# Optimization experiments

Hardware: AMD Instinct MI355X
Metric: run time of the kernel (lower is better)

Reference implementation:

```python
import jax, jax.numpy as jnp
import numpy as np

IN_SHAPE = 4096
H_S = 250        # sender_hidden
H_R = 100        # receiver_hidden
MAX_LEN = 30     # message_shape[0]
VOCAB = 40       # message_shape[1]; EOS = VOCAB-1
OUT_CLS = 512 ** 2  # out_shape[1] ** out_shape[0]


def lstm_cell(x, h, c, W_ih, W_hh, b_ih, b_hh):
    # PyTorch LSTM cell: gate order i, f, g, o
    gates = W_ih @ x + b_ih + W_hh @ h + b_hh
    i, f, g, o = jnp.split(gates, 4)
    c_new = jax.nn.sigmoid(f) * c + jax.nn.sigmoid(i) * jnp.tanh(g)
    h_new = jax.nn.sigmoid(o) * jnp.tanh(c_new)
    return h_new, c_new


def setup_inputs() -> dict:
    key = jax.random.key(0)
    ks = jax.random.split(key, 16)
    s = 0.05
    return {
        "x": jax.random.normal(ks[0], (IN_SHAPE,), dtype=jnp.float32),
        "gumbel_noise": jax.random.gumbel(ks[1], (MAX_LEN, VOCAB), dtype=jnp.float32),
        "W_s1": jax.random.normal(ks[2], (H_S, IN_SHAPE)) * s,
        "b_s1": jnp.zeros((H_S,), jnp.float32),
        "W_ih1": jax.random.normal(ks[3], (4 * H_S, VOCAB)) * s,
        "W_hh1": jax.random.normal(ks[4], (4 * H_S, H_S)) * s,
        "b_ih1": jnp.zeros((4 * H_S,), jnp.float32),
        "b_hh1": jnp.zeros((4 * H_S,), jnp.float32),
        "W_p": jax.random.normal(ks[5], (VOCAB, H_S)) * s,
        "b_p": jnp.zeros((VOCAB,), jnp.float32),
        "W_ih2": jax.random.normal(ks[6], (4 * H_R, VOCAB)) * s,
        "W_hh2": jax.random.normal(ks[7], (4 * H_R, H_R)) * s,
        "b_ih2": jnp.zeros((4 * H_R,), jnp.float32),
        "b_hh2": jnp.zeros((4 * H_R,), jnp.float32),
        "W_r": jax.random.normal(ks[8], (OUT_CLS, H_R)) * s,
        "b_r": jnp.zeros((OUT_CLS,), jnp.float32),
    }


def reference(x, gumbel_noise, W_s1, b_s1, W_ih1, W_hh1, b_ih1, b_hh1,
              W_p, b_p, W_ih2, W_hh2, b_ih2, b_hh2, W_r, b_r):
    dt = x.dtype
    eos = jax.nn.one_hot(VOCAB - 1, VOCAB, dtype=dt)
    # sender: h0 = relu(sender1(x)), c0 = 0, first input = sos = zeros
    h0 = jax.nn.relu(W_s1 @ x + b_s1)
    c0 = jnp.zeros((H_S,), dt)
    sos = jnp.zeros((VOCAB,), dt)
    is_last = jnp.arange(MAX_LEN) == MAX_LEN - 1

    def sender_step(carry, inp):
        h, c, sym, done = carry
        g, last = inp
        nh, nc = lstm_cell(sym, h, c, W_ih1, W_hh1, b_ih1, b_hh1)
        logits = W_p @ nh + b_p
        soft = jax.nn.softmax(logits + g)  # gumbel_softmax, tau=1
        idx = jnp.argmax(soft)
        hard = jax.nn.one_hot(idx, VOCAB, dtype=dt)
        st = hard + soft - jax.lax.stop_gradient(soft)  # straight-through
        # at max length the original appends the plain EOS constant
        emit = jnp.where(last & ~done, eos, st)
        emit = jnp.where(done, eos, emit)
        valid = ~done  # this symbol is part of the message
        new_done = done | (idx == VOCAB - 1) | last
        h = jnp.where(done, h, nh)
        c = jnp.where(done, c, nc)
        sym = jnp.where(done, sym, emit)
        return (h, c, sym, new_done), (emit, valid)

    _, (msg, valid) = jax.lax.scan(
        sender_step, (h0, c0, sos, jnp.array(False)), (gumbel_noise, is_last))

    # receiver LSTM: consume message up to and including first EOS (freeze after)
    def recv_step(carry, inp):
        h, c = carry
        sym, v = inp
        nh, nc = lstm_cell(sym, h, c, W_ih2, W_hh2, b_ih2, b_hh2)
        return (jnp.where(v, nh, h), jnp.where(v, nc, c)), None

    (hR, _), _ = jax.lax.scan(
        recv_step, (jnp.zeros((H_R,), dt), jnp.zeros((H_R,), dt)), (msg, valid))
    return jax.nn.softmax(W_r @ hR + b_r)  # [OUT_CLS]
```

## Files before the change

kernel.cpp:

```cpp
#include <hip/hip_runtime.h>
#include <math.h>

#define HS    250
#define HRr   100
#define VOC   40
#define TMAX  30
#define NCLS  262144
#define KS    10
#define RPB   25

typedef unsigned long long ull;

#define PKNH(wsp, par) ((ull*)(wsp) + (size_t)(par) * 256)
#define PKLP(wsp, par) ((ull*)(wsp) + 512 + (size_t)(par) * 400)
#define PKMSG(wsp)     ((ull*)(wsp) + 1312)
#define WS_SUMS 5024
#define WS_HR   5088
#define WS_ZERO_BYTES 20352

#define AST(p, v) __hip_atomic_store((p), (v), __ATOMIC_RELAXED, __HIP_MEMORY_SCOPE_AGENT)
#define ALD(p)    __hip_atomic_load((p), __ATOMIC_RELAXED, __HIP_MEMORY_SCOPE_AGENT)

__device__ __forceinline__ float sigf(float x) { return 1.f / (1.f + expf(-x)); }
__device__ __forceinline__ float lanebc(float v, int l) {
  return __int_as_float(__builtin_amdgcn_readlane(__float_as_int(v), l));
}
__device__ __forceinline__ ull packtv(unsigned tag, float v) {
  return ((ull)tag << 32) | (ull)__float_as_uint(v);
}
__device__ __forceinline__ float lowf(ull w) { return __uint_as_float((unsigned)w); }

#define SENDER_GATES(P, HV)                                   \
  {                                                           \
    _Pragma("unroll")                                         \
    for (int i = 0; i < 64; i += 4) {                         \
      a0 += whh[i    ] * lanebc(HV, i    );                   \
      a1 += whh[i + 1] * lanebc(HV, i + 1);                   \
      a2 += whh[i + 2] * lanebc(HV, i + 2);                   \
      a3 += whh[i + 3] * lanebc(HV, i + 3);                   \
    }                                                         \
    _Pragma("unroll")                                         \
    for (int i = 0; i < 10; i += 2) {                         \
      a0 += wih[i    ] * lanebc(sv, (P) * 10 + i    );        \
      a1 += wih[i + 1] * lanebc(sv, (P) * 10 + i + 1);        \
    }                                                         \
  }

#define RED(x) ((part[(x)] + part[100 + (x)]) + (part[200 + (x)] + part[300 + (x)]))

__global__ __launch_bounds__(512, 2) void k_sender(
    const float* __restrict__ x,
    const float* __restrict__ W_s1,  const float* __restrict__ b_s1,
    const float* __restrict__ gum,
    const float* __restrict__ W_ih1, const float* __restrict__ W_hh1,
    const float* __restrict__ b_ih1, const float* __restrict__ b_hh1,
    const float* __restrict__ W_p,   const float* __restrict__ b_p,
    const float* __restrict__ W_ih2, const float* __restrict__ W_hh2,
    const float* __restrict__ b_ih2, const float* __restrict__ b_hh2,
    float* __restrict__ ws) {
  __shared__ float part[400];
  __shared__ float h0L[32];
  __shared__ float hx[256];
  __shared__ float lpx[400];
  __shared__ float symx[VOC];
  __shared__ int   doneL;
  __shared__ float gL[400];
  __shared__ float hL[HRr];

  const int b    = blockIdx.x;
  const int t0   = threadIdx.x;
  const int lane = t0 & 63;
  const int w    = t0 >> 6;

  if (b < KS) {
    const int p    = w & 3;
    const int lr   = ((w >> 2) << 6) + lane;
    const bool gact = (lr < 100);
    const int gi   = lr / 25, rr = lr % 25;
    const int grow = gi * 250 + b * RPB + rr;

    float whh[64], wih[10], bsum = 0.f;
    if (gact) {
      #pragma unroll
      for (int i = 0; i < 64; i++) {
        int k = p * 64 + i;
        whh[i] = (k < HS) ? W_hh1[(size_t)grow * HS + k] : 0.f;
      }
      #pragma unroll
      for (int i = 0; i < 10; i++) wih[i] = W_ih1[grow * VOC + p * 10 + i];
      bsum = b_ih1[grow] + b_hh1[grow];
    }
    float wps[RPB];
    if (w == 0) {
      #pragma unroll
      for (int r = 0; r < RPB; r++)
        wps[r] = (lane < VOC) ? W_p[lane * HS + b * RPB + r] : 0.f;
    }
    const float bpv = (lane < VOC) ? b_p[lane] : 0.f;

    {
      const int nr = (w == 7) ? 4 : 3;
      for (int j = 0; j < nr; ++j) {
        const int r = 3 * w + j;
        const float4* wr = (const float4*)(W_s1 + (size_t)(b * RPB + r) * 4096);
        const float4* xr = (const float4*)x;
        float a0 = 0.f, a1 = 0.f, a2 = 0.f, a3 = 0.f;
        #pragma unroll
        for (int q = 0; q < 16; ++q) {
          float4 w4 = wr[lane + (q << 6)], x4 = xr[lane + (q << 6)];
          a0 += w4.x * x4.x; a1 += w4.y * x4.y; a2 += w4.z * x4.z; a3 += w4.w * x4.w;
        }
        float acc = (a0 + a1) + (a2 + a3);
        #pragma unroll
        for (int o = 32; o; o >>= 1) acc += __shfl_down(acc, o);
        if (lane == 0) h0L[r] = acc + b_s1[b * RPB + r];
      }
    }
    __syncthreads();
    if (w == 0 && lane < RPB) {
      float hn0 = fmaxf(h0L[lane], 0.f);
      AST(&PKNH(ws, 1)[b * RPB + lane], packtv(1u, hn0));
    }

    float c  = 0.f;
    float sv = 0.f;
    const bool h3v = (192 + lane) < HS;
    const bool l6v = lane < (400 - 384);

    for (int s = 0; s <= TMAX; ++s) {
      float gv = 0.f;
      if (s > 0 && lane < VOC) gv = gum[(s - 1) * VOC + lane];

      if (w == 0) {
        const unsigned need = (unsigned)(s + 1);
        const int par = (s + 1) & 1;
        const ull* nhp = PKNH(ws, par);
        const ull* lpp = PKLP(ws, par);
        const bool lpact = (s > 0);
        const ull dummy = (ull)need << 32;
        ull hw0, hw1, hw2, hw3;
        ull lw0 = 0, lw1 = 0, lw2 = 0, lw3 = 0, lw4 = 0, lw5 = 0, lw6 = 0;
        for (;;) {
          hw0 = ALD(&nhp[lane]);
          hw1 = ALD(&nhp[64 + lane]);
          hw2 = ALD(&nhp[128 + lane]);
          hw3 = h3v ? ALD(&nhp[192 + lane]) : dummy;
          bool ok = (unsigned)(hw0 >> 32) == need && (unsigned)(hw1 >> 32) == need &&
                    (unsigned)(hw2 >> 32) == need && (unsigned)(hw3 >> 32) == need;
          if (lpact) {
            lw0 = ALD(&lpp[lane]);        lw1 = ALD(&lpp[64 + lane]);
            lw2 = ALD(&lpp[128 + lane]);  lw3 = ALD(&lpp[192 + lane]);
            lw4 = ALD(&lpp[256 + lane]);  lw5 = ALD(&lpp[320 + lane]);
            lw6 = l6v ? ALD(&lpp[384 + lane]) : dummy;
            ok = ok && (unsigned)(lw0 >> 32) == need && (unsigned)(lw1 >> 32) == need &&
                       (unsigned)(lw2 >> 32) == need && (unsigned)(lw3 >> 32) == need &&
                       (unsigned)(lw4 >> 32) == need && (unsigned)(lw5 >> 32) == need &&
                       (unsigned)(lw6 >> 32) == need;
          }
          if (__all(ok)) break;
        }
        hx[lane] = lowf(hw0); hx[64 + lane] = lowf(hw1); hx[128 + lane] = lowf(hw2);
        if (h3v) hx[192 + lane] = lowf(hw3);
        if (lpact) {
          lpx[lane] = lowf(lw0);        lpx[64 + lane] = lowf(lw1);
          lpx[128 + lane] = lowf(lw2);  lpx[192 + lane] = lowf(lw3);
          lpx[256 + lane] = lowf(lw4);  lpx[320 + lane] = lowf(lw5);
          if (l6v) lpx[384 + lane] = lowf(lw6);
        }
      }
      __syncthreads();

      float hv0 = hx[lane], hv1 = hx[64 + lane], hv2 = hx[128 + lane];
      float hv3 = h3v ? hx[192 + lane] : 0.f;

      if (s > 0) {
        float lg = -INFINITY;
        if (lane < VOC) {
          float acc = bpv + gv;
          #pragma unroll
          for (int m = 0; m < KS; ++m) acc += lpx[m * VOC + lane];
          lg = acc;
        }
        float v = lg; int bi = lane;
        #pragma unroll
        for (int o = 32; o; o >>= 1) {
          float ov = __shfl_down(v, o);
          int   oi = __shfl_down(bi, o);
          if (ov > v) { v = ov; bi = oi; }
        }
        float m  = __shfl(v, 0);
        int  idx = __shfl(bi, 0);
        float e = (lane < VOC) ? expf(lg - m) : 0.f;
        float ssum = e;
        #pragma unroll
        for (int o = 32; o; o >>= 1) ssum += __shfl_down(ssum, o);
        ssum = __shfl(ssum, 0);
        float soft = e / ssum;
        float hard = (lane == idx) ? 1.f : 0.f;
        float st   = (hard + soft) - soft;
        const bool last = (s - 1 == TMAX - 1);
        float emit = last ? ((lane == VOC - 1) ? 1.f : 0.f) : st;
        const bool done = (idx == VOC - 1) || last;
        if (b == 0 && w == 0 && lane < VOC)
          AST(&PKMSG(ws)[(s - 1) * VOC + lane],
              packtv((unsigned)s | (done ? 0x10000u : 0u), emit));
        sv = (lane < VOC) ? emit : 0.f;
        if (done) break;
      }

      if (gact) {
        float a0 = bsum, a1 = 0.f, a2 = 0.f, a3 = 0.f;
        if      (p == 0) SENDER_GATES(0, hv0)
        else if (p == 1) SENDER_GATES(1, hv1)
        else if (p == 2) SENDER_GATES(2, hv2)
        else             SENDER_GATES(3, hv3)
        part[p * 100 + lr] = (a0 + a1) + (a2 + a3);
      }
      __syncthreads();

      if (w == 0) {
        float gi_ = RED(lane < RPB ? lane : 0);
        float gf_ = RED(25 + (lane < RPB ? lane : 0));
        float gg_ = RED(50 + (lane < RPB ? lane : 0));
        float go_ = RED(75 + (lane < RPB ? lane : 0));
        float ig = sigf(gi_), fg = sigf(gf_), gg = tanhf(gg_), og = sigf(go_);
        float cn = fg * c + ig * gg; c = cn;
        float hn = og * tanhf(cn);
        float lpsum = 0.f;
        #pragma unroll
        for (int r = 0; r < RPB; ++r) lpsum += wps[r] * lanebc(hn, r);
        const unsigned nt = (unsigned)(s + 2);
        const int np = (s + 2) & 1;
        if (lane < RPB) AST(&PKNH(ws, np)[b * RPB + lane], packtv(nt, hn));
        if (lane < VOC) AST(&PKLP(ws, np)[b * VOC + lane], packtv(nt, lpsum));
      }
    }
  } else {
    const bool act = (t0 < 400);
    float wih2[VOC], whh2[HRr], bsum2 = 0.f;
    if (act) {
      #pragma unroll
      for (int i = 0; i < VOC; i++) wih2[i] = W_ih2[t0 * VOC + i];
      #pragma unroll
      for (int i = 0; i < HRr; i++) whh2[i] = W_hh2[t0 * HRr + i];
      bsum2 = b_ih2[t0] + b_hh2[t0];
    }
    float c2 = 0.f, rv0 = 0.f, rv1 = 0.f;

    for (int t = 0; t < TMAX; ++t) {
      if (w == 0) {
        const bool mv = (lane < VOC);
        ull mw = 0;
        for (;;) {
          if (mv) mw = ALD(&PKMSG(ws)[t * VOC + lane]);
          bool ok = !mv || ((unsigned)(mw >> 32) & 0xFFFFu) == (unsigned)(t + 1);
          if (__all(ok)) break;
        }
        if (mv) symx[lane] = lowf(mw);
        if (lane == 0) doneL = (int)(((unsigned)(mw >> 32)) >> 16);
      }
      __syncthreads();
      const bool done = (doneL != 0);
      float sv2 = (lane < VOC) ? symx[lane] : 0.f;
      if (act) {
        float a0 = bsum2, a1 = 0.f, a2 = 0.f, a3 = 0.f;
        #pragma unroll
        for (int i = 0; i < VOC; i += 4) {
          a0 += wih2[i    ] * lanebc(sv2, i    );
          a1 += wih2[i + 1] * lanebc(sv2, i + 1);
          a2 += wih2[i + 2] * lanebc(sv2, i + 2);
          a3 += wih2[i + 3] * lanebc(sv2, i + 3);
        }
        #pragma unroll
        for (int i = 0; i < 64; i += 4) {
          a0 += whh2[i    ] * lanebc(rv0, i    );
          a1 += whh2[i + 1] * lanebc(rv0, i + 1);
          a2 += whh2[i + 2] * lanebc(rv0, i + 2);
          a3 += whh2[i + 3] * lanebc(rv0, i + 3);
        }
        #pragma unroll
        for (int i = 0; i < 36; i += 4) {
          a0 += whh2[64 + i    ] * lanebc(rv1, i    );
          a1 += whh2[64 + i + 1] * lanebc(rv1, i + 1);
          a2 += whh2[64 + i + 2] * lanebc(rv1, i + 2);
          a3 += whh2[64 + i + 3] * lanebc(rv1, i + 3);
        }
        gL[t0] = (a0 + a1) + (a2 + a3);
      }
      __syncthreads();
      if (t0 < HRr) {
        float ig = sigf(gL[t0]);
        float fg = sigf(gL[100 + t0]);
        float gg = tanhf(gL[200 + t0]);
        float og = sigf(gL[300 + t0]);
        float cn = fg * c2 + ig * gg; c2 = cn;
        hL[t0] = og * tanhf(cn);
      }
      __syncthreads();
      rv0 = hL[lane];
      rv1 = (lane < 36) ? hL[64 + lane] : 0.f;
      if (done) break;
    }
    if (t0 < HRr) ws[WS_HR + t0] = hL[t0];
  }
}

__global__ __launch_bounds__(256) void k_out(
    const float* __restrict__ W_r, const float* __restrict__ b_r,
    float* __restrict__ ws, float* __restrict__ out) {
  __shared__ float4 h4[25];
  __shared__ float  red[4];
  const int t0 = threadIdx.x;
  if (t0 < 25) h4[t0] = ((const float4*)(ws + WS_HR))[t0];
  __syncthreads();
  const int lane = t0 & 63;
  const int wv   = t0 >> 6;
  const int sl   = lane & 31;
  const int hf   = lane >> 5;
  const int base = blockIdx.x * 128 + wv * 32;
  float accs = 0.f;
  #pragma unroll 4
  for (int i = 0; i < 16; ++i) {
    const int row = base + 2 * i + hf;
    float v = 0.f;
    if (sl < 25) {
      float4 w4 = ((const float4*)W_r)[(size_t)row * 25 + sl];
      float4 hq = h4[sl];
      v = w4.x * hq.x + w4.y * hq.y + w4.z * hq.z + w4.w * hq.w;
    }
    #pragma unroll
    for (int o = 16; o; o >>= 1) v += __shfl_down(v, o, 32);
    float e = 0.f;
    if (sl == 0) { e = expf(v + b_r[row]); accs += e; }
    float eB = __shfl(e, 32);
    if (lane == 0) ((float2*)out)[(base + 2 * i) >> 1] = make_float2(e, eB);
  }
  accs += __shfl_down(accs, 32);
  if (lane == 0) red[wv] = accs;
  __syncthreads();
  if (t0 == 0)
    atomicAdd(&ws[WS_SUMS + (blockIdx.x & 63)], (red[0] + red[1]) + (red[2] + red[3]));
}

__global__ __launch_bounds__(256) void k_scale(const float* __restrict__ ws,
                                               float* __restrict__ out) {
  float s = ws[WS_SUMS + (threadIdx.x & 63)];
  #pragma unroll
  for (int o = 1; o < 64; o <<= 1) s += __shfl_xor(s, o);
  const float rinv = 1.f / s;
  const int i = blockIdx.x * 256 + threadIdx.x;
  float4 e = ((const float4*)out)[i];
  e.x *= rinv; e.y *= rinv; e.z *= rinv; e.w *= rinv;
  ((float4*)out)[i] = e;
}

extern "C" void kernel_launch(void* const* d_in, const int* in_sizes, int n_in,
                              void* d_out, int out_size, void* d_ws, size_t ws_size,
                              hipStream_t stream) {
  const float* x     = (const float*)d_in[0];
  const float* gum   = (const float*)d_in[1];
  const float* W_s1  = (const float*)d_in[2];
  const float* b_s1  = (const float*)d_in[3];
  const float* W_ih1 = (const float*)d_in[4];
  const float* W_hh1 = (const float*)d_in[5];
  const float* b_ih1 = (const float*)d_in[6];
  const float* b_hh1 = (const float*)d_in[7];
  const float* W_p   = (const float*)d_in[8];
  const float* b_p   = (const float*)d_in[9];
  const float* W_ih2 = (const float*)d_in[10];
  const float* W_hh2 = (const float*)d_in[11];
  const float* b_ih2 = (const float*)d_in[12];
  const float* b_hh2 = (const float*)d_in[13];
  const float* W_r   = (const float*)d_in[14];
  const float* b_r   = (const float*)d_in[15];
  float* ws  = (float*)d_ws;
  float* out = (float*)d_out;

  (void)hipMemsetAsync(d_ws, 0, WS_ZERO_BYTES, stream);
  k_sender<<<KS + 1,   512, 0, stream>>>(x, W_s1, b_s1, gum, W_ih1, W_hh1,
                                         b_ih1, b_hh1, W_p, b_p,
                                         W_ih2, W_hh2, b_ih2, b_hh2, ws);
  k_out   <<<NCLS/128, 256, 0, stream>>>(W_r, b_r, ws, out);
  k_scale <<<NCLS/1024,256, 0, stream>>>(ws, out);
}
```

Measured before the change: 313.4 us.

## Co-locate sender blocks on one XCC and exchange step data through its L2

```diff
diff --git a/kernel.cpp b/kernel.cpp
--- a/kernel.cpp
+++ b/kernel.cpp
@@ -8,18 +8,27 @@
 #define NCLS  262144
 #define KS    10
 #define RPB   25
+#define NROLE (KS + 1)
+#define GRID_SENDER 256
+#define SPIN_CAP 400
 
 typedef unsigned long long ull;
 
-#define PKNH(wsp, par) ((ull*)(wsp) + (size_t)(par) * 256)
-#define PKLP(wsp, par) ((ull*)(wsp) + 512 + (size_t)(par) * 400)
-#define PKMSG(wsp)     ((ull*)(wsp) + 1312)
+#define PKNH(wsp, par)  ((ull*)(wsp) + (size_t)(par) * 256)
+#define PKLP(wsp, par)  ((ull*)(wsp) + 512 + (size_t)(par) * 400)
+#define PKMSG(wsp)      ((ull*)(wsp) + 1312)
+#define PKNHS(wsp, par) ((ull*)(wsp) + 2600 + (size_t)(par) * 256)
+#define PKLPS(wsp, par) ((ull*)(wsp) + 3112 + (size_t)(par) * 400)
+#define PKMSGS(wsp)     ((ull*)(wsp) + 3912)
 #define WS_SUMS 5024
 #define WS_HR   5088
-#define WS_ZERO_BYTES 20352
+#define CTRL_LEADER(wsp) ((unsigned*)((char*)(wsp) + 40896))
+#define CTRL_ROLE(wsp)   ((unsigned*)((char*)(wsp) + 40900))
+#define WS_ZERO_BYTES 40912
 
 #define AST(p, v) __hip_atomic_store((p), (v), __ATOMIC_RELAXED, __HIP_MEMORY_SCOPE_AGENT)
 #define ALD(p)    __hip_atomic_load((p), __ATOMIC_RELAXED, __HIP_MEMORY_SCOPE_AGENT)
+#define TG(wv)    ((unsigned)((wv) >> 32))
 
 __device__ __forceinline__ float sigf(float x) { return 1.f / (1.f + expf(-x)); }
 __device__ __forceinline__ float lanebc(float v, int l) {
@@ -29,6 +38,17 @@
   return ((ull)tag << 32) | (ull)__float_as_uint(v);
 }
 __device__ __forceinline__ float lowf(ull w) { return __uint_as_float((unsigned)w); }
+
+__device__ __forceinline__ ull ld_l2(const ull* p) {
+  ull r;
+  asm volatile("global_load_dwordx2 %0, %1, off sc0\n\t"
+               "s_waitcnt vmcnt(0)"
+               : "=v"(r) : "v"(p) : "memory");
+  return r;
+}
+__device__ __forceinline__ void st_l2(ull* p, ull v) {
+  asm volatile("global_store_dwordx2 %0, %1, off sc0" :: "v"(p), "v"(v) : "memory");
+}
 
 #define SENDER_GATES(P, HV)                                   \
   {                                                           \
@@ -66,11 +86,38 @@
   __shared__ int   doneL;
   __shared__ float gL[400];
   __shared__ float hL[HRr];
-
-  const int b    = blockIdx.x;
+  __shared__ int   roleL;
+
   const int t0   = threadIdx.x;
   const int lane = t0 & 63;
   const int w    = t0 >> 6;
+
+  unsigned xcc;
+  asm volatile("s_getreg_b32 %0, hwreg(HW_REG_XCC_ID)" : "=s"(xcc));
+  if (t0 == 0) {
+    unsigned old = atomicCAS(CTRL_LEADER(ws), 0u, xcc + 1u);
+    unsigned leader = (old == 0u) ? xcc : (old - 1u);
+    int r = -1;
+    if (xcc == leader) {
+      unsigned rr = atomicAdd(CTRL_ROLE(ws), 1u);
+      if (rr < NROLE) r = (int)rr;
+    } else {
+      bool filled = false;
+      for (int it = 0; it < 48; ++it) {
+        __builtin_amdgcn_s_sleep(32);
+        if (__hip_atomic_load(CTRL_ROLE(ws), __ATOMIC_RELAXED,
+                              __HIP_MEMORY_SCOPE_AGENT) >= NROLE) { filled = true; break; }
+      }
+      if (!filled) {
+        unsigned rr = atomicAdd(CTRL_ROLE(ws), 1u);
+        if (rr < NROLE) r = (int)rr;
+      }
+    }
+    roleL = r;
+  }
+  __syncthreads();
+  const int b = roleL;
+  if (b < 0) return;
 
   if (b < KS) {
     const int p    = w & 3;
@@ -119,11 +166,14 @@
     __syncthreads();
     if (w == 0 && lane < RPB) {
       float hn0 = fmaxf(h0L[lane], 0.f);
-      AST(&PKNH(ws, 1)[b * RPB + lane], packtv(1u, hn0));
+      ull wv = packtv(1u, hn0);
+      st_l2(&PKNH(ws, 1)[b * RPB + lane], wv);
+      AST(&PKNHS(ws, 1)[b * RPB + lane], wv);
     }
 
     float c  = 0.f;
     float sv = 0.f;
+    bool useLLC = false;
     const bool h3v = (192 + lane) < HS;
     const bool l6v = lane < (400 - 384);
 
@@ -134,30 +184,64 @@
       if (w == 0) {
         const unsigned need = (unsigned)(s + 1);
         const int par = (s + 1) & 1;
-        const ull* nhp = PKNH(ws, par);
-        const ull* lpp = PKLP(ws, par);
+        const ull* nhp  = PKNH(ws, par);
+        const ull* lpp  = PKLP(ws, par);
+        const ull* nhps = PKNHS(ws, par);
+        const ull* lpps = PKLPS(ws, par);
         const bool lpact = (s > 0);
         const ull dummy = (ull)need << 32;
+        const ull* pn0 = nhp + lane;        const ull* pn1 = nhp + 64 + lane;
+        const ull* pn2 = nhp + 128 + lane;  const ull* pn3 = nhp + 192 + lane;
+        const ull* pl0 = lpp + lane;        const ull* pl1 = lpp + 64 + lane;
+        const ull* pl2 = lpp + 128 + lane;  const ull* pl3 = lpp + 192 + lane;
+        const ull* pl4 = lpp + 256 + lane;  const ull* pl5 = lpp + 320 + lane;
+        const ull* pl6 = lpp + 384 + lane;
         ull hw0, hw1, hw2, hw3;
         ull lw0 = 0, lw1 = 0, lw2 = 0, lw3 = 0, lw4 = 0, lw5 = 0, lw6 = 0;
+        int spins = 0;
         for (;;) {
-          hw0 = ALD(&nhp[lane]);
-          hw1 = ALD(&nhp[64 + lane]);
-          hw2 = ALD(&nhp[128 + lane]);
-          hw3 = h3v ? ALD(&nhp[192 + lane]) : dummy;
-          bool ok = (unsigned)(hw0 >> 32) == need && (unsigned)(hw1 >> 32) == need &&
-                    (unsigned)(hw2 >> 32) == need && (unsigned)(hw3 >> 32) == need;
+          if (!useLLC) {
+            asm volatile(
+              "global_load_dwordx2 %0, %11, off sc0\n\t"
+              "global_load_dwordx2 %1, %12, off sc0\n\t"
+              "global_load_dwordx2 %2, %13, off sc0\n\t"
+              "global_load_dwordx2 %3, %14, off sc0\n\t"
+              "global_load_dwordx2 %4, %15, off sc0\n\t"
+              "global_load_dwordx2 %5, %16, off sc0\n\t"
+              "global_load_dwordx2 %6, %17, off sc0\n\t"
+              "global_load_dwordx2 %7, %18, off sc0\n\t"
+              "global_load_dwordx2 %8, %19, off sc0\n\t"
+              "global_load_dwordx2 %9, %20, off sc0\n\t"
+              "global_load_dwordx2 %10, %21, off sc0\n\t"
+              "s_waitcnt vmcnt(0)"
+              : "=&v"(hw0), "=&v"(hw1), "=&v"(hw2), "=&v"(hw3),
+                "=&v"(lw0), "=&v"(lw1), "=&v"(lw2), "=&v"(lw3),
+                "=&v"(lw4), "=&v"(lw5), "=&v"(lw6)
+              : "v"(pn0), "v"(pn1), "v"(pn2), "v"(pn3),
+                "v"(pl0), "v"(pl1), "v"(pl2), "v"(pl3),
+                "v"(pl4), "v"(pl5), "v"(pl6)
+              : "memory");
+          } else {
+            hw0 = ALD(&nhps[lane]);
+            hw1 = ALD(&nhps[64 + lane]);
+            hw2 = ALD(&nhps[128 + lane]);
+            hw3 = h3v ? ALD(&nhps[192 + lane]) : dummy;
+            if (lpact) {
+              lw0 = ALD(&lpps[lane]);        lw1 = ALD(&lpps[64 + lane]);
+              lw2 = ALD(&lpps[128 + lane]);  lw3 = ALD(&lpps[192 + lane]);
+              lw4 = ALD(&lpps[256 + lane]);  lw5 = ALD(&lpps[320 + lane]);
+              lw6 = l6v ? ALD(&lpps[384 + lane]) : dummy;
+            }
+          }
+          bool ok = TG(hw0) == need && TG(hw1) == need && TG(hw2) == need &&
+                    (!h3v || TG(hw3) == need);
           if (lpact) {
-            lw0 = ALD(&lpp[lane]);        lw1 = ALD(&lpp[64 + lane]);
-            lw2 = ALD(&lpp[128 + lane]);  lw3 = ALD(&lpp[192 + lane]);
-            lw4 = ALD(&lpp[256 + lane]);  lw5 = ALD(&lpp[320 + lane]);
-            lw6 = l6v ? ALD(&lpp[384 + lane]) : dummy;
-            ok = ok && (unsigned)(lw0 >> 32) == need && (unsigned)(lw1 >> 32) == need &&
-                       (unsigned)(lw2 >> 32) == need && (unsigned)(lw3 >> 32) == need &&
-                       (unsigned)(lw4 >> 32) == need && (unsigned)(lw5 >> 32) == need &&
-                       (unsigned)(lw6 >> 32) == need;
+            ok = ok && TG(lw0) == need && TG(lw1) == need && TG(lw2) == need &&
+                       TG(lw3) == need && TG(lw4) == need && TG(lw5) == need &&
+                       (!l6v || TG(lw6) == need);
           }
           if (__all(ok)) break;
+          if (!useLLC && ++spins > SPIN_CAP) useLLC = true;
         }
         hx[lane] = lowf(hw0); hx[64 + lane] = lowf(hw1); hx[128 + lane] = lowf(hw2);
         if (h3v) hx[192 + lane] = lowf(hw3);
@@ -201,9 +285,11 @@
         const bool last = (s - 1 == TMAX - 1);
         float emit = last ? ((lane == VOC - 1) ? 1.f : 0.f) : st;
         const bool done = (idx == VOC - 1) || last;
-        if (b == 0 && w == 0 && lane < VOC)
-          AST(&PKMSG(ws)[(s - 1) * VOC + lane],
-              packtv((unsigned)s | (done ? 0x10000u : 0u), emit));
+        if (b == 0 && w == 0 && lane < VOC) {
+          ull mv_ = packtv((unsigned)s | (done ? 0x10000u : 0u), emit);
+          st_l2(&PKMSG(ws)[(s - 1) * VOC + lane], mv_);
+          AST(&PKMSGS(ws)[(s - 1) * VOC + lane], mv_);
+        }
         sv = (lane < VOC) ? emit : 0.f;
         if (done) break;
       }
@@ -231,8 +317,16 @@
         for (int r = 0; r < RPB; ++r) lpsum += wps[r] * lanebc(hn, r);
         const unsigned nt = (unsigned)(s + 2);
         const int np = (s + 2) & 1;
-        if (lane < RPB) AST(&PKNH(ws, np)[b * RPB + lane], packtv(nt, hn));
-        if (lane < VOC) AST(&PKLP(ws, np)[b * VOC + lane], packtv(nt, lpsum));
+        if (lane < RPB) {
+          ull wv = packtv(nt, hn);
+          st_l2(&PKNH(ws, np)[b * RPB + lane], wv);
+          AST(&PKNHS(ws, np)[b * RPB + lane], wv);
+        }
+        if (lane < VOC) {
+          ull wl = packtv(nt, lpsum);
+          st_l2(&PKLP(ws, np)[b * VOC + lane], wl);
+          AST(&PKLPS(ws, np)[b * VOC + lane], wl);
+        }
       }
     }
   } else {
@@ -246,15 +340,19 @@
       bsum2 = b_ih2[t0] + b_hh2[t0];
     }
     float c2 = 0.f, rv0 = 0.f, rv1 = 0.f;
+    bool useLLC = false;
 
     for (int t = 0; t < TMAX; ++t) {
       if (w == 0) {
         const bool mv = (lane < VOC);
         ull mw = 0;
+        int spins = 0;
         for (;;) {
-          if (mv) mw = ALD(&PKMSG(ws)[t * VOC + lane]);
+          if (mv) mw = useLLC ? ALD(&PKMSGS(ws)[t * VOC + lane])
+                              : ld_l2(&PKMSG(ws)[t * VOC + lane]);
           bool ok = !mv || ((unsigned)(mw >> 32) & 0xFFFFu) == (unsigned)(t + 1);
           if (__all(ok)) break;
+          if (!useLLC && ++spins > SPIN_CAP) useLLC = true;
         }
         if (mv) symx[lane] = lowf(mw);
         if (lane == 0) doneL = (int)(((unsigned)(mw >> 32)) >> 16);
@@ -377,9 +475,9 @@
   float* out = (float*)d_out;
 
   (void)hipMemsetAsync(d_ws, 0, WS_ZERO_BYTES, stream);
-  k_sender<<<KS + 1,   512, 0, stream>>>(x, W_s1, b_s1, gum, W_ih1, W_hh1,
-                                         b_ih1, b_hh1, W_p, b_p,
-                                         W_ih2, W_hh2, b_ih2, b_hh2, ws);
+  k_sender<<<GRID_SENDER, 512, 0, stream>>>(x, W_s1, b_s1, gum, W_ih1, W_hh1,
+                                            b_ih1, b_hh1, W_p, b_p,
+                                            W_ih2, W_hh2, b_ih2, b_hh2, ws);
   k_out   <<<NCLS/128, 256, 0, stream>>>(W_r, b_r, ws, out);
   k_scale <<<NCLS/1024,256, 0, stream>>>(ws, out);
 }
```

Result: slower. 446.7 us (+42.5%).

## Fuse output projection into sender kernel and prefetch W_r during recurrence

Applied to the files above, without the earlier changes.

```diff
diff --git a/kernel.cpp b/kernel.cpp
--- a/kernel.cpp
+++ b/kernel.cpp
@@ -8,6 +8,9 @@
 #define NCLS  262144
 #define KS    10
 #define RPB   25
+#define GRID  256
+#define NOUT  (GRID - KS - 1)
+#define NCHUNK (NCLS / 256)
 
 typedef unsigned long long ull;
 
@@ -16,7 +19,8 @@
 #define PKMSG(wsp)     ((ull*)(wsp) + 1312)
 #define WS_SUMS 5024
 #define WS_HR   5088
-#define WS_ZERO_BYTES 20352
+#define WS_HRTAG(wsp) ((unsigned*)((char*)(wsp) + 20752))
+#define WS_ZERO_BYTES 20768
 
 #define AST(p, v) __hip_atomic_store((p), (v), __ATOMIC_RELAXED, __HIP_MEMORY_SCOPE_AGENT)
 #define ALD(p)    __hip_atomic_load((p), __ATOMIC_RELAXED, __HIP_MEMORY_SCOPE_AGENT)
@@ -48,7 +52,7 @@
 
 #define RED(x) ((part[(x)] + part[100 + (x)]) + (part[200 + (x)] + part[300 + (x)]))
 
-__global__ __launch_bounds__(512, 2) void k_sender(
+__global__ __launch_bounds__(512, 2) void k_mega(
     const float* __restrict__ x,
     const float* __restrict__ W_s1,  const float* __restrict__ b_s1,
     const float* __restrict__ gum,
@@ -57,7 +61,8 @@
     const float* __restrict__ W_p,   const float* __restrict__ b_p,
     const float* __restrict__ W_ih2, const float* __restrict__ W_hh2,
     const float* __restrict__ b_ih2, const float* __restrict__ b_hh2,
-    float* __restrict__ ws) {
+    const float* __restrict__ W_r,   const float* __restrict__ b_r,
+    float* __restrict__ ws,          float* __restrict__ out) {
   __shared__ float part[400];
   __shared__ float h0L[32];
   __shared__ float hx[256];
@@ -66,6 +71,9 @@
   __shared__ int   doneL;
   __shared__ float gL[400];
   __shared__ float hL[HRr];
+  __shared__ float hfs[HRr];
+  __shared__ float4 h4[25];
+  __shared__ float  red8[8];
 
   const int b    = blockIdx.x;
   const int t0   = threadIdx.x;
@@ -235,7 +243,7 @@
         if (lane < VOC) AST(&PKLP(ws, np)[b * VOC + lane], packtv(nt, lpsum));
       }
     }
-  } else {
+  } else if (b == KS) {
     const bool act = (t0 < 400);
     float wih2[VOC], whh2[HRr], bsum2 = 0.f;
     if (act) {
@@ -302,44 +310,69 @@
       if (done) break;
     }
     if (t0 < HRr) ws[WS_HR + t0] = hL[t0];
+    __syncthreads();
+    if (t0 == 0)
+      __hip_atomic_store(WS_HRTAG(ws), 1u, __ATOMIC_RELEASE,
+                         __HIP_MEMORY_SCOPE_AGENT);
+  } else {
+    const int o = b - KS - 1;
+    float dummy = 0.f;
+    const float4* wr4 = (const float4*)W_r;
+    for (int c = o; c < NCHUNK; c += NOUT) {
+      const int f0 = c * 6400;
+      for (int i = f0 + t0; i < f0 + 6400; i += 512) {
+        float4 w4 = wr4[i];
+        dummy += (w4.x + w4.y) + (w4.z + w4.w);
+      }
+    }
+    asm volatile("" :: "v"(dummy));
+
+    if (t0 == 0) {
+      while (__hip_atomic_load(WS_HRTAG(ws), __ATOMIC_ACQUIRE,
+                               __HIP_MEMORY_SCOPE_AGENT) == 0u)
+        __builtin_amdgcn_s_sleep(16);
+    }
+    __syncthreads();
+    if (t0 < HRr)
+      hfs[t0] = __uint_as_float(ALD((const unsigned*)(ws + WS_HR) + t0));
+    __syncthreads();
+    if (t0 < 25)
+      h4[t0] = make_float4(hfs[4*t0], hfs[4*t0+1], hfs[4*t0+2], hfs[4*t0+3]);
+    __syncthreads();
+
+    const int sub = t0 >> 8;
+    const int tl  = t0 & 255;
+    const int wv  = tl >> 6;
+    const int sl  = lane & 31;
+    const int hf  = lane >> 5;
+    float accs = 0.f;
+    for (int c = o; c < NCHUNK; c += NOUT) {
+      const int base = c * 256 + sub * 128 + wv * 32;
+      #pragma unroll 4
+      for (int i = 0; i < 16; ++i) {
+        const int row = base + 2 * i + hf;
+        float v = 0.f;
+        if (sl < 25) {
+          float4 w4 = wr4[(size_t)row * 25 + sl];
+          float4 hq = h4[sl];
+          v = w4.x * hq.x + w4.y * hq.y + w4.z * hq.z + w4.w * hq.w;
+        }
+        #pragma unroll
+        for (int off = 16; off; off >>= 1) v += __shfl_down(v, off, 32);
+        float e = 0.f;
+        if (sl == 0) { e = expf(v + b_r[row]); accs += e; }
+        float eB = __shfl(e, 32);
+        if (lane == 0) ((float2*)out)[(base + 2 * i) >> 1] = make_float2(e, eB);
+      }
+    }
+    accs += __shfl_down(accs, 32);
+    if (lane == 0) red8[w] = accs;
+    __syncthreads();
+    if (t0 == 0)
+      atomicAdd(&ws[WS_SUMS + (b & 63)],
+                ((red8[0] + red8[1]) + (red8[2] + red8[3])) +
+                ((red8[4] + red8[5]) + (red8[6] + red8[7])));
   }
-}
-
-__global__ __launch_bounds__(256) void k_out(
-    const float* __restrict__ W_r, const float* __restrict__ b_r,
-    float* __restrict__ ws, float* __restrict__ out) {
-  __shared__ float4 h4[25];
-  __shared__ float  red[4];
-  const int t0 = threadIdx.x;
-  if (t0 < 25) h4[t0] = ((const float4*)(ws + WS_HR))[t0];
-  __syncthreads();
-  const int lane = t0 & 63;
-  const int wv   = t0 >> 6;
-  const int sl   = lane & 31;
-  const int hf   = lane >> 5;
-  const int base = blockIdx.x * 128 + wv * 32;
-  float accs = 0.f;
-  #pragma unroll 4
-  for (int i = 0; i < 16; ++i) {
-    const int row = base + 2 * i + hf;
-    float v = 0.f;
-    if (sl < 25) {
-      float4 w4 = ((const float4*)W_r)[(size_t)row * 25 + sl];
-      float4 hq = h4[sl];
-      v = w4.x * hq.x + w4.y * hq.y + w4.z * hq.z + w4.w * hq.w;
-    }
-    #pragma unroll
-    for (int o = 16; o; o >>= 1) v += __shfl_down(v, o, 32);
-    float e = 0.f;
-    if (sl == 0) { e = expf(v + b_r[row]); accs += e; }
-    float eB = __shfl(e, 32);
-    if (lane == 0) ((float2*)out)[(base + 2 * i) >> 1] = make_float2(e, eB);
-  }
-  accs += __shfl_down(accs, 32);
-  if (lane == 0) red[wv] = accs;
-  __syncthreads();
-  if (t0 == 0)
-    atomicAdd(&ws[WS_SUMS + (blockIdx.x & 63)], (red[0] + red[1]) + (red[2] + red[3]));
 }
 
 __global__ __launch_bounds__(256) void k_scale(const float* __restrict__ ws,
@@ -377,9 +410,9 @@
   float* out = (float*)d_out;
 
   (void)hipMemsetAsync(d_ws, 0, WS_ZERO_BYTES, stream);
-  k_sender<<<KS + 1,   512, 0, stream>>>(x, W_s1, b_s1, gum, W_ih1, W_hh1,
-                                         b_ih1, b_hh1, W_p, b_p,
-                                         W_ih2, W_hh2, b_ih2, b_hh2, ws);
-  k_out   <<<NCLS/128, 256, 0, stream>>>(W_r, b_r, ws, out);
-  k_scale <<<NCLS/1024,256, 0, stream>>>(ws, out);
+  k_mega <<<GRID, 512, 0, stream>>>(x, W_s1, b_s1, gum, W_ih1, W_hh1,
+                                    b_ih1, b_hh1, W_p, b_p,
+                                    W_ih2, W_hh2, b_ih2, b_hh2,
+                                    W_r, b_r, ws, out);
+  k_scale<<<NCLS/1024, 256, 0, stream>>>(ws, out);
 }
```

New measurement: 497.9 us. +58.9%, slower.

## Fuse softmax scaling into output GEMV via grid barrier and LDS-transposed tiles

Applied to the files above, without the earlier changes.

```diff
diff --git a/kernel.cpp b/kernel.cpp
--- a/kernel.cpp
+++ b/kernel.cpp
@@ -9,6 +9,12 @@
 #define KS    10
 #define RPB   25
 
+#define OB    512
+#define ORPB  (NCLS / OB)
+#define OTIL  128
+#define NTIL  (ORPB / OTIL)
+#define LDST  129
+
 typedef unsigned long long ull;
 
 #define PKNH(wsp, par) ((ull*)(wsp) + (size_t)(par) * 256)
@@ -16,7 +22,8 @@
 #define PKMSG(wsp)     ((ull*)(wsp) + 1312)
 #define WS_SUMS 5024
 #define WS_HR   5088
-#define WS_ZERO_BYTES 20352
+#define CTRL_DONE(wsp) ((unsigned*)((char*)(wsp) + 20752))
+#define WS_ZERO_BYTES 20756
 
 #define AST(p, v) __hip_atomic_store((p), (v), __ATOMIC_RELAXED, __HIP_MEMORY_SCOPE_AGENT)
 #define ALD(p)    __hip_atomic_load((p), __ATOMIC_RELAXED, __HIP_MEMORY_SCOPE_AGENT)
@@ -305,53 +312,86 @@
   }
 }
 
-__global__ __launch_bounds__(256) void k_out(
+__global__ __launch_bounds__(256) void k_out2(
     const float* __restrict__ W_r, const float* __restrict__ b_r,
     float* __restrict__ ws, float* __restrict__ out) {
-  __shared__ float4 h4[25];
-  __shared__ float  red[4];
-  const int t0 = threadIdx.x;
-  if (t0 < 25) h4[t0] = ((const float4*)(ws + WS_HR))[t0];
+  __shared__ float ldsT[100 * LDST];
+  __shared__ float hsh[HRr];
+  __shared__ float part2[OTIL];
+  __shared__ float redw[2];
+
+  const int t0   = threadIdx.x;
+  const int lane = t0 & 63;
+  const int w    = t0 >> 6;
+  const int b    = blockIdx.x;
+
+  if (t0 < HRr) hsh[t0] = ws[WS_HR + t0];
   __syncthreads();
-  const int lane = t0 & 63;
-  const int wv   = t0 >> 6;
-  const int sl   = lane & 31;
-  const int hf   = lane >> 5;
-  const int base = blockIdx.x * 128 + wv * 32;
+
+  const float4* wr4 = (const float4*)W_r;
+  const int rloc  = t0 & (OTIL - 1);
+  const int khalf = (t0 >> 7) * 50;
   float accs = 0.f;
-  #pragma unroll 4
-  for (int i = 0; i < 16; ++i) {
-    const int row = base + 2 * i + hf;
-    float v = 0.f;
-    if (sl < 25) {
-      float4 w4 = ((const float4*)W_r)[(size_t)row * 25 + sl];
-      float4 hq = h4[sl];
-      v = w4.x * hq.x + w4.y * hq.y + w4.z * hq.z + w4.w * hq.w;
-    }
+
+  for (int tile = 0; tile < NTIL; ++tile) {
+    const int row0 = b * ORPB + tile * OTIL;
     #pragma unroll
-    for (int o = 16; o; o >>= 1) v += __shfl_down(v, o, 32);
-    float e = 0.f;
-    if (sl == 0) { e = expf(v + b_r[row]); accs += e; }
-    float eB = __shfl(e, 32);
-    if (lane == 0) ((float2*)out)[(base + 2 * i) >> 1] = make_float2(e, eB);
+    for (int it = 0; it < 13; ++it) {
+      const int j = t0 + it * 256;
+      if (j < OTIL * 25) {
+        float4 v = wr4[(size_t)row0 * 25 + j];
+        const int r = j / 25, c = j % 25;
+        float* p = &ldsT[(4 * c) * LDST + r];
+        p[0]        = v.x;
+        p[LDST]     = v.y;
+        p[2 * LDST] = v.z;
+        p[3 * LDST] = v.w;
+      }
+    }
+    __syncthreads();
+    float a0 = 0.f, a1 = 0.f;
+    #pragma unroll
+    for (int k = 0; k < 50; k += 2) {
+      a0 += ldsT[(khalf + k    ) * LDST + rloc] * hsh[khalf + k    ];
+      a1 += ldsT[(khalf + k + 1) * LDST + rloc] * hsh[khalf + k + 1];
+    }
+    const float acc = a0 + a1;
+    if (t0 >= OTIL) part2[rloc] = acc;
+    __syncthreads();
+    if (t0 < OTIL) {
+      const int row = row0 + t0;
+      float e = expf(acc + part2[t0] + b_r[row]);
+      out[row] = e;
+      accs += e;
+    }
+    __syncthreads();
   }
-  accs += __shfl_down(accs, 32);
-  if (lane == 0) red[wv] = accs;
+
+  float s = accs;
+  #pragma unroll
+  for (int o = 32; o; o >>= 1) s += __shfl_down(s, o);
+  if (lane == 0 && w < 2) redw[w] = s;
   __syncthreads();
-  if (t0 == 0)
-    atomicAdd(&ws[WS_SUMS + (blockIdx.x & 63)], (red[0] + red[1]) + (red[2] + red[3]));
-}
-
-__global__ __launch_bounds__(256) void k_scale(const float* __restrict__ ws,
-                                               float* __restrict__ out) {
-  float s = ws[WS_SUMS + (threadIdx.x & 63)];
+  if (t0 == 0) {
+    atomicAdd(&ws[WS_SUMS + (b & 63)], redw[0] + redw[1]);
+    __hip_atomic_fetch_add(CTRL_DONE(ws), 1u, __ATOMIC_RELEASE,
+                           __HIP_MEMORY_SCOPE_AGENT);
+    while (__hip_atomic_load(CTRL_DONE(ws), __ATOMIC_RELAXED,
+                             __HIP_MEMORY_SCOPE_AGENT) < (unsigned)OB)
+      __builtin_amdgcn_s_sleep(4);
+  }
+  __syncthreads();
+
+  float ssum = __uint_as_float(ALD((const unsigned*)(ws + WS_SUMS) + (lane & 63)));
   #pragma unroll
-  for (int o = 1; o < 64; o <<= 1) s += __shfl_xor(s, o);
-  const float rinv = 1.f / s;
-  const int i = blockIdx.x * 256 + threadIdx.x;
-  float4 e = ((const float4*)out)[i];
-  e.x *= rinv; e.y *= rinv; e.z *= rinv; e.w *= rinv;
-  ((float4*)out)[i] = e;
+  for (int off = 1; off < 64; off <<= 1) ssum += __shfl_xor(ssum, off);
+  const float rinv = 1.f / ssum;
+  if (t0 < 128) {
+    float4* po = (float4*)out;
+    float4 e = po[b * 128 + t0];
+    e.x *= rinv; e.y *= rinv; e.z *= rinv; e.w *= rinv;
+    po[b * 128 + t0] = e;
+  }
 }
 
 extern "C" void kernel_launch(void* const* d_in, const int* in_sizes, int n_in,
@@ -377,9 +417,8 @@
   float* out = (float*)d_out;
 
   (void)hipMemsetAsync(d_ws, 0, WS_ZERO_BYTES, stream);
-  k_sender<<<KS + 1,   512, 0, stream>>>(x, W_s1, b_s1, gum, W_ih1, W_hh1,
-                                         b_ih1, b_hh1, W_p, b_p,
-                                         W_ih2, W_hh2, b_ih2, b_hh2, ws);
-  k_out   <<<NCLS/128, 256, 0, stream>>>(W_r, b_r, ws, out);
-  k_scale <<<NCLS/1024,256, 0, stream>>>(ws, out);
+  k_sender<<<KS + 1, 512, 0, stream>>>(x, W_s1, b_s1, gum, W_ih1, W_hh1,
+                                       b_ih1, b_hh1, W_p, b_p,
+                                       W_ih2, W_hh2, b_ih2, b_hh2, ws);
+  k_out2  <<<OB,     256, 0, stream>>>(W_r, b_r, ws, out);
 }
```

Result: slower. 346.7 us (+10.6%).
